# Kernel optimization log

Measured on AMD Instinct MI355X. Metric: run time of the kernel, lower is better.

The kernel has to match this reference:

```python
import jax, jax.numpy as jnp
import numpy as np

D_IN = 1024
D_OUT = 1024
H = 16            # head_cnt
G = 4             # attention_groups
LF = 2            # linformer_factor
HEAD_OUT = D_OUT // H          # 64 (value head dim)
DQ = HEAD_OUT // LF            # 32 (query/key head dim)
B, T = 2, 2048


def setup_inputs() -> dict:
    key = jax.random.key(0)
    ks = jax.random.split(key, 7)
    s = 0.02
    return {
        "x": jax.random.normal(ks[0], (B, T, D_IN), dtype=jnp.float32),
        "Wq": jax.random.normal(ks[1], (D_IN, D_OUT // LF), dtype=jnp.float32) * s,
        "Wk": jax.random.normal(ks[2], (D_IN, (D_OUT // LF) // G), dtype=jnp.float32) * s,
        "Wv": jax.random.normal(ks[3], (D_IN, D_OUT // G), dtype=jnp.float32) * s,
        "Wp": jax.random.normal(ks[4], (D_OUT, D_OUT), dtype=jnp.float32) * s,
        "bp": jnp.zeros((D_OUT,), dtype=jnp.float32),
    }


def _alibi_bias(T, dtype):
    # standard ALiBi slopes for H heads (H is a power of 2): m_h = 2^(-8h/H), h=1..H
    slopes = jnp.asarray(2.0 ** (-8.0 * np.arange(1, H + 1) / H), dtype=dtype)
    pos = jnp.arange(T)
    rel = (pos[None, :] - pos[:, None]).astype(dtype)  # j - i, <= 0 on causal part
    return slopes[:, None, None] * rel[None, :, :]      # (H, T, T)


def reference(x, Wq, Wk, Wv, Wp, bp):
    b, t, _ = x.shape
    q = x @ Wq                                  # (b, t, D_OUT/LF)
    k = jnp.tile(x @ Wk, (1, 1, G))             # repeat KV groups -> (b, t, D_OUT/LF)
    v = jnp.tile(x @ Wv, (1, 1, G))             # (b, t, D_OUT)

    q = q.reshape(b, t, H, DQ).transpose(0, 2, 1, 3)        # (b, H, t, DQ)
    k = k.reshape(b, t, H, DQ).transpose(0, 2, 1, 3)
    v = v.reshape(b, t, H, HEAD_OUT).transpose(0, 2, 1, 3)  # (b, H, t, HEAD_OUT)

    scores = jnp.einsum('bhqd,bhkd->bhqk', q, k)            # (b, H, t, t)
    causal = jnp.triu(jnp.ones((t, t), dtype=bool), k=1)
    scores = jnp.where(causal, -jnp.inf, scores)
    # faithful to source: alibi added after masking, then scaled by 1/sqrt(d_k)
    scores = (scores + _alibi_bias(t, scores.dtype)) / jnp.sqrt(jnp.asarray(DQ, scores.dtype))
    w = jax.nn.softmax(scores, axis=-1)
    ctx = jnp.einsum('bhqk,bhkd->bqhd', w, v).reshape(b, t, D_OUT)
    return ctx @ Wp + bp
```

## Files before the change

kernel.cpp:

```cpp
#include <hip/hip_runtime.h>
#include <hip/hip_bf16.h>

#define T_SEQ 2048
#define H_CNT 16
#define B_SZ  2
#define QKV_LD 896
#define KOFF   512
#define VOFF   640

typedef float  f32x4   __attribute__((ext_vector_type(4)));
typedef float  f32x16  __attribute__((ext_vector_type(16)));
typedef __bf16 bf16x8  __attribute__((ext_vector_type(8)));

static __device__ __forceinline__ ushort f2bf(float f) {
    union { float f; unsigned u; } v; v.f = f;
    unsigned u = v.u;
    unsigned r = (u + 0x7fffu + ((u >> 16) & 1u)) >> 16;
    return (ushort)r;
}
static __device__ __forceinline__ unsigned pack2bf(float a, float b) {
    union { __bf16 h[2]; unsigned u; } pk;
    pk.h[0] = (__bf16)a; pk.h[1] = (__bf16)b;
    return pk.u;
}

static __device__ __forceinline__ f32x4 mfma16(bf16x8 a, bf16x8 b, f32x4 c) {
    return __builtin_amdgcn_mfma_f32_16x16x32_bf16(a, b, c, 0, 0, 0);
}
static __device__ __forceinline__ f32x16 mfma32(bf16x8 a, bf16x8 b, f32x16 c) {
    return __builtin_amdgcn_mfma_f32_32x32x16_bf16(a, b, c, 0, 0, 0);
}

static __device__ __forceinline__ void gl_lds16(const void* g, void* l) {
    __builtin_amdgcn_global_load_lds((const __attribute__((address_space(1))) void*)g,
                                     (__attribute__((address_space(3))) void*)l, 16, 0, 0);
}

__global__ __launch_bounds__(256) void convert_bf16(const float* __restrict__ src,
                                                    ushort* __restrict__ dst) {
    const int i = blockIdx.x * 256 + threadIdx.x;
    const float4 v0 = reinterpret_cast<const float4*>(src)[i * 2];
    const float4 v1 = reinterpret_cast<const float4*>(src)[i * 2 + 1];
    uint4 o;
    o.x = (unsigned)f2bf(v0.x) | ((unsigned)f2bf(v0.y) << 16);
    o.y = (unsigned)f2bf(v0.z) | ((unsigned)f2bf(v0.w) << 16);
    o.z = (unsigned)f2bf(v1.x) | ((unsigned)f2bf(v1.y) << 16);
    o.w = (unsigned)f2bf(v1.z) | ((unsigned)f2bf(v1.w) << 16);
    reinterpret_cast<uint4*>(dst)[i] = o;
}

__global__ __launch_bounds__(256) void prep_weights(const float* __restrict__ Wq,
                                                    const float* __restrict__ Wk,
                                                    const float* __restrict__ Wv,
                                                    const float* __restrict__ Wp,
                                                    ushort* __restrict__ Wqkvt,
                                                    ushort* __restrict__ Wpt) {
    __shared__ float tile[32][33];
    const int x = blockIdx.x;
    const float* src; ushort* dst; int C, cx;
    if (x < 16)      { src = Wq; dst = Wqkvt;              C = 512;  cx = x; }
    else if (x < 20) { src = Wk; dst = Wqkvt + 512 * 1024; C = 128;  cx = x - 16; }
    else if (x < 28) { src = Wv; dst = Wqkvt + 640 * 1024; C = 256;  cx = x - 20; }
    else             { src = Wp; dst = Wpt;                C = 1024; cx = x - 28; }
    const int tx = threadIdx.x & 31, ty = threadIdx.x >> 5;
    const int r0 = blockIdx.y * 32, c0 = cx * 32;
#pragma unroll
    for (int i = 0; i < 32; i += 8)
        tile[ty + i][tx] = src[(size_t)(r0 + ty + i) * C + c0 + tx];
    __syncthreads();
#pragma unroll
    for (int i = 0; i < 32; i += 8)
        dst[(size_t)(c0 + ty + i) * 1024 + r0 + tx] = f2bf(tile[tx][ty + i]);
}

__global__ __launch_bounds__(256) void transpose_bf16_str(const ushort* __restrict__ src,
                                                          int src_ld, size_t src_zoff,
                                                          ushort* __restrict__ dst,
                                                          int R, int C, size_t dst_zoff) {
    __shared__ ushort tile[32][33];
    const int tx = threadIdx.x & 31, ty = threadIdx.x >> 5;
    const int r0 = blockIdx.y * 32, c0 = blockIdx.x * 32;
    const ushort* s = src + (size_t)blockIdx.z * src_zoff;
    ushort* d = dst + (size_t)blockIdx.z * dst_zoff;
#pragma unroll
    for (int i = 0; i < 32; i += 8)
        tile[ty + i][tx] = s[(size_t)(r0 + ty + i) * src_ld + c0 + tx];
    __syncthreads();
#pragma unroll
    for (int i = 0; i < 32; i += 8)
        d[(size_t)(c0 + ty + i) * R + r0 + tx] = tile[tx][ty + i];
}

template <bool OUT_BF16>
__global__ __launch_bounds__(256) void gemm_bf16(const ushort* __restrict__ A,
                                                 const ushort* __restrict__ Bt,
                                                 const float* __restrict__ bias,
                                                 void* __restrict__ Cout,
                                                 int M, int N, int K) {
    __shared__ __align__(16) ushort As[64 * 32];
    __shared__ __align__(16) ushort Bs[128 * 32];

    const int tid = threadIdx.x;
    const int w = tid >> 6, l = tid & 63;
    const int bm = blockIdx.y * 64, bn = blockIdx.x * 128;
    const int wr = (w >> 1) * 32, wc = (w & 1) * 64;
    const int lr = l & 15, lk = (l >> 4) * 8;
    const int crow = l >> 2, ck8 = (l & 3) * 8;

    const ushort* Ag0 = A + (size_t)(bm + w * 16 + crow) * K + ck8;
    const ushort* Bg0 = Bt + (size_t)(bn + w * 16 + crow) * K + ck8;
    const ushort* Bg1 = Bt + (size_t)(bn + (w + 4) * 16 + crow) * K + ck8;
    ushort* Al0 = &As[w * 16 * 32];
    ushort* Bl0 = &Bs[w * 16 * 32];
    ushort* Bl1 = &Bs[(w + 4) * 16 * 32];

    f32x4 acc[2][4];
#pragma unroll
    for (int m = 0; m < 2; ++m)
#pragma unroll
        for (int n = 0; n < 4; ++n) acc[m][n] = (f32x4){0.f, 0.f, 0.f, 0.f};

    for (int k0 = 0; k0 < K; k0 += 32) {
        __syncthreads();
        gl_lds16(Ag0 + k0, Al0);
        gl_lds16(Bg0 + k0, Bl0);
        gl_lds16(Bg1 + k0, Bl1);
        __syncthreads();

        bf16x8 af[2], bfr[4];
#pragma unroll
        for (int m = 0; m < 2; ++m)
            af[m] = *reinterpret_cast<const bf16x8*>(&As[(wr + m * 16 + lr) * 32 + lk]);
#pragma unroll
        for (int n = 0; n < 4; ++n)
            bfr[n] = *reinterpret_cast<const bf16x8*>(&Bs[(wc + n * 16 + lr) * 32 + lk]);
#pragma unroll
        for (int m = 0; m < 2; ++m)
#pragma unroll
            for (int n = 0; n < 4; ++n)
                acc[m][n] = mfma16(af[m], bfr[n], acc[m][n]);
    }

    const int orow = bm + wr + (l >> 4) * 4;
    const int ocol0 = bn + wc + lr;
#pragma unroll
    for (int m = 0; m < 2; ++m)
#pragma unroll
        for (int n = 0; n < 4; ++n) {
            const int col = ocol0 + n * 16;
            const float bv = OUT_BF16 ? 0.0f : bias[col];
#pragma unroll
            for (int r = 0; r < 4; ++r) {
                const size_t idx = (size_t)(orow + m * 16 + r) * N + col;
                if constexpr (OUT_BF16)
                    reinterpret_cast<ushort*>(Cout)[idx] = f2bf(acc[m][n][r]);
                else
                    reinterpret_cast<float*>(Cout)[idx] = acc[m][n][r] + bv;
            }
        }
}

#define LDK 40
#define LDV 72

__global__ __launch_bounds__(512) void attn_mfma7(const ushort* __restrict__ qkv,
                                                  const ushort* __restrict__ vT,
                                                  ushort* __restrict__ ctx) {
    __shared__ __align__(16) ushort Ks[2][64 * LDK];
    __shared__ __align__(16) ushort Vs[2][64 * LDV];
    __shared__ float lsred[4][32];

    const int tid = threadIdx.x;
    const int w = tid >> 6, l = tid & 63;
    const int lq = l & 31;
    const int hi = l >> 5;
    const int tp = blockIdx.x, g = blockIdx.y, b = blockIdx.z;
    const int hd = w & 3, grp = w >> 2;
    const int h = g + 4 * hd;

    const float slope = exp2f(-0.5f * (float)(h + 1));
    const float k1 = 0.17677669529663687f * 1.4426950408889634f;
    const float k2 = slope * k1;
    const int Wint = (int)(275.0f / slope);

    const int st = tid & 255;
    const int sd = st >> 2;
    const int c4 = st & 3;
    const int sc8 = c4 * 8;
    const int voff = (c4 & 1) * 4 + (c4 >> 1) * 16;
    const ushort* kgp = qkv + (size_t)b * T_SEQ * QKV_LD + KOFF + g * 32 + (size_t)sd * QKV_LD + sc8;
    const ushort* vgp = vT + ((size_t)b * 256 + g * 64 + sd) * T_SEQ;

    float* red = reinterpret_cast<float*>(&Vs[0][0]);

    int cur = 0;
    for (int ph = 0; ph < 2; ++ph) {
        const int t = ph ? tp : (63 - tp);
        const int i0 = t * 32;
        const int nkeys = i0 + 32;
        const int jtmax = (nkeys + 63) & ~63;

        const ushort* qrow = qkv + ((size_t)(b * T_SEQ + i0 + lq)) * QKV_LD + h * 32 + hi * 8;
        const bf16x8 qa = *reinterpret_cast<const bf16x8*>(qrow);
        const bf16x8 qb = *reinterpret_cast<const bf16x8*>(qrow + 16);

        f32x16 o0, o1;
#pragma unroll
        for (int r = 0; r < 16; ++r) { o0[r] = 0.0f; o1[r] = 0.0f; }
        float ls = 0.0f;

        uint4 kreg, vr0, vr1;
        if (tid < 256) {
            kreg = *reinterpret_cast<const uint4*>(kgp);
        } else {
            vr0 = *reinterpret_cast<const uint4*>(vgp + sc8);
            vr1 = *reinterpret_cast<const uint4*>(vgp + 32 + sc8);
        }

        for (int jt = 0; jt < jtmax; jt += 64) {
            if (tid < 256) {
                *reinterpret_cast<uint4*>(&Ks[cur][sd * LDK + sc8]) = kreg;
            } else {
                uint2 lo0 = make_uint2(vr0.x, vr0.y), hi0v = make_uint2(vr0.z, vr0.w);
                uint2 lo1 = make_uint2(vr1.x, vr1.y), hi1v = make_uint2(vr1.z, vr1.w);
                *reinterpret_cast<uint2*>(&Vs[cur][sd * LDV + voff]) = lo0;
                *reinterpret_cast<uint2*>(&Vs[cur][sd * LDV + voff + 8]) = hi0v;
                *reinterpret_cast<uint2*>(&Vs[cur][sd * LDV + 32 + voff]) = lo1;
                *reinterpret_cast<uint2*>(&Vs[cur][sd * LDV + 32 + voff + 8]) = hi1v;
            }
            const int jn = jt + 64;
            if (jn < jtmax) {
                if (tid < 256) {
                    kreg = *reinterpret_cast<const uint4*>(kgp + (size_t)jn * QKV_LD);
                } else {
                    vr0 = *reinterpret_cast<const uint4*>(vgp + jn + sc8);
                    vr1 = *reinterpret_cast<const uint4*>(vgp + jn + 32 + sc8);
                }
            }
            __syncthreads();

            const int jts = jt + 32 * grp;
            if (jts < nkeys && jts + 31 >= i0 - Wint) {
                const bf16x8 ka = *reinterpret_cast<const bf16x8*>(&Ks[cur][(32 * grp + lq) * LDK + hi * 8]);
                const bf16x8 kb2 = *reinterpret_cast<const bf16x8*>(&Ks[cur][(32 * grp + lq) * LDK + 16 + hi * 8]);
                f32x16 p;
#pragma unroll
                for (int r = 0; r < 16; ++r) p[r] = 0.0f;
                __builtin_amdgcn_s_setprio(1);
                p = mfma32(ka, qa, p);
                p = mfma32(kb2, qb, p);
                __builtin_amdgcn_s_setprio(0);

                const int dlt = jts + 4 * hi - i0 - lq;
                const float base2 = k2 * (float)dlt;
                float pe[16];
                if (jts + 31 > i0) {
#pragma unroll
                    for (int r = 0; r < 16; ++r) {
                        const int off = (r & 3) + 8 * (r >> 2);
                        const float arg = fmaf(p[r], k1, fmaf((float)off, k2, base2));
                        float e = exp2f(arg);
                        if (dlt + off > 0) e = 0.0f;
                        ls += e;
                        pe[r] = e;
                    }
                } else {
#pragma unroll
                    for (int r = 0; r < 16; ++r) {
                        const int off = (r & 3) + 8 * (r >> 2);
                        const float arg = fmaf(p[r], k1, fmaf((float)off, k2, base2));
                        const float e = exp2f(arg);
                        ls += e;
                        pe[r] = e;
                    }
                }
                union { unsigned u[4]; bf16x8 v; } A1, A2;
#pragma unroll
                for (int j2 = 0; j2 < 4; ++j2) A1.u[j2] = pack2bf(pe[2 * j2], pe[2 * j2 + 1]);
#pragma unroll
                for (int j2 = 0; j2 < 4; ++j2) A2.u[j2] = pack2bf(pe[8 + 2 * j2], pe[9 + 2 * j2]);

                const int vr0i = lq * LDV + 32 * grp;
                const int vr1i = (32 + lq) * LDV + 32 * grp;
                const bf16x8 v00 = *reinterpret_cast<const bf16x8*>(&Vs[cur][vr0i + hi * 8]);
                const bf16x8 v01 = *reinterpret_cast<const bf16x8*>(&Vs[cur][vr0i + 16 + hi * 8]);
                const bf16x8 v10 = *reinterpret_cast<const bf16x8*>(&Vs[cur][vr1i + hi * 8]);
                const bf16x8 v11 = *reinterpret_cast<const bf16x8*>(&Vs[cur][vr1i + 16 + hi * 8]);
                __builtin_amdgcn_s_setprio(1);
                o0 = mfma32(A1.v, v00, o0);
                o0 = mfma32(A2.v, v01, o0);
                o1 = mfma32(A1.v, v10, o1);
                o1 = mfma32(A2.v, v11, o1);
                __builtin_amdgcn_s_setprio(0);
            }
            cur ^= 1;
        }

        const float ls2 = ls + __shfl_xor(ls, 32);
        __syncthreads();
        if (grp == 0) {
#pragma unroll
            for (int r = 0; r < 16; ++r) red[hd * 1024 + l * 16 + r] = o0[r];
            if (hi == 0) lsred[hd][lq] = ls2;
        }
        __syncthreads();
        float inv = 0.0f;
        if (grp == 1) {
#pragma unroll
            for (int r = 0; r < 16; ++r) o0[r] += red[hd * 1024 + l * 16 + r];
            inv = 1.0f / (ls2 + lsred[hd][lq]);
        }
        __syncthreads();
        if (grp == 0) {
#pragma unroll
            for (int r = 0; r < 16; ++r) red[hd * 1024 + l * 16 + r] = o1[r];
        }
        __syncthreads();
        if (grp == 1) {
#pragma unroll
            for (int r = 0; r < 16; ++r) o1[r] += red[hd * 1024 + l * 16 + r];
#pragma unroll
            for (int r = 0; r < 16; ++r) {
                const int qr = (r & 3) + 8 * (r >> 2) + 4 * hi;
                const float invq = __shfl(inv, qr);
                const size_t row = (size_t)(b * T_SEQ + i0 + qr);
                ctx[row * 1024 + h * 64 + lq] = f2bf(o0[r] * invq);
                ctx[row * 1024 + h * 64 + 32 + lq] = f2bf(o1[r] * invq);
            }
        }
        __syncthreads();
    }
}

extern "C" void kernel_launch(void* const* d_in, const int* in_sizes, int n_in,
                              void* d_out, int out_size, void* d_ws, size_t ws_size,
                              hipStream_t stream) {
    const float* x  = (const float*)d_in[0];
    const float* Wq = (const float*)d_in[1];
    const float* Wk = (const float*)d_in[2];
    const float* Wv = (const float*)d_in[3];
    const float* Wp = (const float*)d_in[4];
    const float* bp = (const float*)d_in[5];

    const int M = B_SZ * T_SEQ;

    ushort* ws    = (ushort*)d_ws;
    ushort* xb    = ws;
    ushort* Wqkvt = xb + 4194304;
    ushort* Wpt   = Wqkvt + 917504;
    ushort* qkv   = Wpt + 1048576;
    ushort* vTb   = qkv + 3670016;
    ushort* cbuf  = vTb + 1048576;

    convert_bf16<<<2048, 256, 0, stream>>>(x, xb);
    prep_weights<<<dim3(60, 32), 256, 0, stream>>>(Wq, Wk, Wv, Wp, Wqkvt, Wpt);

    gemm_bf16<true><<<dim3(7, 64), 256, 0, stream>>>(xb, Wqkvt, nullptr, qkv, M, 896, 1024);

    transpose_bf16_str<<<dim3(8, 64, 2), 256, 0, stream>>>(
        qkv + VOFF, QKV_LD, (size_t)T_SEQ * QKV_LD, vTb, T_SEQ, 256, (size_t)256 * T_SEQ);

    attn_mfma7<<<dim3(32, 4, B_SZ), 512, 0, stream>>>(qkv, vTb, cbuf);

    gemm_bf16<false><<<dim3(8, 64), 256, 0, stream>>>(cbuf, Wpt, bp, (float*)d_out, M, 1024, 1024);
}
```

Measured before the change: 100.5 us.

## Widen attention to 16 waves with 4-way key split; double GEMM k-step

The attention kernel now launches 1024 threads per block. Each head's key range is split across four wave groups using 128-key tiles, with a three-slot LDS reduction for the partial outputs and row sums. This raises in-flight waves per CU, since the grid only fills about one block per CU. The GEMM loads two 32-wide K slices per barrier pair, halving sync count per K. The costs are higher reduction overhead and more idle waves on short causal rows.

```diff
diff --git a/kernel.cpp b/kernel.cpp
--- a/kernel.cpp
+++ b/kernel.cpp
@@ -97,8 +97,8 @@
                                                  const float* __restrict__ bias,
                                                  void* __restrict__ Cout,
                                                  int M, int N, int K) {
-    __shared__ __align__(16) ushort As[64 * 32];
-    __shared__ __align__(16) ushort Bs[128 * 32];
+    __shared__ __align__(16) ushort Aa[64 * 32], Ab[64 * 32];
+    __shared__ __align__(16) ushort Ba[128 * 32], Bb[128 * 32];
 
     const int tid = threadIdx.x;
     const int w = tid >> 6, l = tid & 63;
@@ -107,12 +107,15 @@
     const int lr = l & 15, lk = (l >> 4) * 8;
     const int crow = l >> 2, ck8 = (l & 3) * 8;
 
-    const ushort* Ag0 = A + (size_t)(bm + w * 16 + crow) * K + ck8;
+    const ushort* Ag  = A + (size_t)(bm + w * 16 + crow) * K + ck8;
     const ushort* Bg0 = Bt + (size_t)(bn + w * 16 + crow) * K + ck8;
     const ushort* Bg1 = Bt + (size_t)(bn + (w + 4) * 16 + crow) * K + ck8;
-    ushort* Al0 = &As[w * 16 * 32];
-    ushort* Bl0 = &Bs[w * 16 * 32];
-    ushort* Bl1 = &Bs[(w + 4) * 16 * 32];
+    ushort* Ala  = &Aa[w * 16 * 32];
+    ushort* Alb  = &Ab[w * 16 * 32];
+    ushort* Bl0a = &Ba[w * 16 * 32];
+    ushort* Bl0b = &Bb[w * 16 * 32];
+    ushort* Bl1a = &Ba[(w + 4) * 16 * 32];
+    ushort* Bl1b = &Bb[(w + 4) * 16 * 32];
 
     f32x4 acc[2][4];
 #pragma unroll
@@ -120,25 +123,34 @@
 #pragma unroll
         for (int n = 0; n < 4; ++n) acc[m][n] = (f32x4){0.f, 0.f, 0.f, 0.f};
 
-    for (int k0 = 0; k0 < K; k0 += 32) {
-        __syncthreads();
-        gl_lds16(Ag0 + k0, Al0);
-        gl_lds16(Bg0 + k0, Bl0);
-        gl_lds16(Bg1 + k0, Bl1);
-        __syncthreads();
-
-        bf16x8 af[2], bfr[4];
+    for (int k0 = 0; k0 < K; k0 += 64) {
+        __syncthreads();
+        gl_lds16(Ag + k0, Ala);
+        gl_lds16(Ag + k0 + 32, Alb);
+        gl_lds16(Bg0 + k0, Bl0a);
+        gl_lds16(Bg0 + k0 + 32, Bl0b);
+        gl_lds16(Bg1 + k0, Bl1a);
+        gl_lds16(Bg1 + k0 + 32, Bl1b);
+        __syncthreads();
+
+        bf16x8 af0[2], af1[2], bf0[4], bf1[4];
+#pragma unroll
+        for (int m = 0; m < 2; ++m) {
+            af0[m] = *reinterpret_cast<const bf16x8*>(&Aa[(wr + m * 16 + lr) * 32 + lk]);
+            af1[m] = *reinterpret_cast<const bf16x8*>(&Ab[(wr + m * 16 + lr) * 32 + lk]);
+        }
+#pragma unroll
+        for (int n = 0; n < 4; ++n) {
+            bf0[n] = *reinterpret_cast<const bf16x8*>(&Ba[(wc + n * 16 + lr) * 32 + lk]);
+            bf1[n] = *reinterpret_cast<const bf16x8*>(&Bb[(wc + n * 16 + lr) * 32 + lk]);
+        }
 #pragma unroll
         for (int m = 0; m < 2; ++m)
-            af[m] = *reinterpret_cast<const bf16x8*>(&As[(wr + m * 16 + lr) * 32 + lk]);
-#pragma unroll
-        for (int n = 0; n < 4; ++n)
-            bfr[n] = *reinterpret_cast<const bf16x8*>(&Bs[(wc + n * 16 + lr) * 32 + lk]);
-#pragma unroll
-        for (int m = 0; m < 2; ++m)
-#pragma unroll
-            for (int n = 0; n < 4; ++n)
-                acc[m][n] = mfma16(af[m], bfr[n], acc[m][n]);
+#pragma unroll
+            for (int n = 0; n < 4; ++n) {
+                acc[m][n] = mfma16(af0[m], bf0[n], acc[m][n]);
+                acc[m][n] = mfma16(af1[m], bf1[n], acc[m][n]);
+            }
     }
 
     const int orow = bm + wr + (l >> 4) * 4;
@@ -161,14 +173,14 @@
 }
 
 #define LDK 40
-#define LDV 72
-
-__global__ __launch_bounds__(512) void attn_mfma7(const ushort* __restrict__ qkv,
-                                                  const ushort* __restrict__ vT,
-                                                  ushort* __restrict__ ctx) {
-    __shared__ __align__(16) ushort Ks[2][64 * LDK];
+#define LDV 136
+
+__global__ __launch_bounds__(1024) void attn_mfma8(const ushort* __restrict__ qkv,
+                                                   const ushort* __restrict__ vT,
+                                                   ushort* __restrict__ ctx) {
+    __shared__ __align__(16) ushort Ks[2][128 * LDK];
     __shared__ __align__(16) ushort Vs[2][64 * LDV];
-    __shared__ float lsred[4][32];
+    __shared__ float lsred[3][4][32];
 
     const int tid = threadIdx.x;
     const int w = tid >> 6, l = tid & 63;
@@ -183,22 +195,28 @@
     const float k2 = slope * k1;
     const int Wint = (int)(275.0f / slope);
 
-    const int st = tid & 255;
-    const int sd = st >> 2;
-    const int c4 = st & 3;
-    const int sc8 = c4 * 8;
-    const int voff = (c4 & 1) * 4 + (c4 >> 1) * 16;
-    const ushort* kgp = qkv + (size_t)b * T_SEQ * QKV_LD + KOFF + g * 32 + (size_t)sd * QKV_LD + sc8;
-    const ushort* vgp = vT + ((size_t)b * 256 + g * 64 + sd) * T_SEQ;
-
-    float* red = reinterpret_cast<float*>(&Vs[0][0]);
+    const int ksd = tid >> 2, kc4 = tid & 3;
+    const ushort* kgp = qkv + (size_t)b * T_SEQ * QKV_LD + KOFF + g * 32 +
+                        (size_t)ksd * QKV_LD + kc4 * 8;
+    const int sv = tid & 511;
+    const int vsd = sv >> 3, vj = sv & 7;
+    const int vs0 = (vj >> 2) << 1, vc4 = vj & 3;
+    const int voff = (vc4 & 1) * 4 + (vc4 >> 1) * 16;
+    const ushort* vgp = vT + ((size_t)b * 256 + g * 64 + vsd) * T_SEQ + vs0 * 32 + vc4 * 8;
+    const int vl0 = vsd * LDV + vs0 * 32 + voff;
+    const int vl1 = vsd * LDV + (vs0 + 1) * 32 + voff;
+
+    float* slotA = reinterpret_cast<float*>(&Ks[0][0]);
+    float* slotB = reinterpret_cast<float*>(&Vs[0][0]);
+    float* slotC = reinterpret_cast<float*>(&Vs[1][0]);
+    const int sidx = (hd * 64 + l) * 16;
 
     int cur = 0;
     for (int ph = 0; ph < 2; ++ph) {
         const int t = ph ? tp : (63 - tp);
         const int i0 = t * 32;
         const int nkeys = i0 + 32;
-        const int jtmax = (nkeys + 63) & ~63;
+        const int jtmax = (nkeys + 127) & ~127;
 
         const ushort* qrow = qkv + ((size_t)(b * T_SEQ + i0 + lq)) * QKV_LD + h * 32 + hi * 8;
         const bf16x8 qa = *reinterpret_cast<const bf16x8*>(qrow);
@@ -210,39 +228,37 @@
         float ls = 0.0f;
 
         uint4 kreg, vr0, vr1;
-        if (tid < 256) {
+        if (tid < 512) {
             kreg = *reinterpret_cast<const uint4*>(kgp);
         } else {
-            vr0 = *reinterpret_cast<const uint4*>(vgp + sc8);
-            vr1 = *reinterpret_cast<const uint4*>(vgp + 32 + sc8);
-        }
-
-        for (int jt = 0; jt < jtmax; jt += 64) {
-            if (tid < 256) {
-                *reinterpret_cast<uint4*>(&Ks[cur][sd * LDK + sc8]) = kreg;
+            vr0 = *reinterpret_cast<const uint4*>(vgp);
+            vr1 = *reinterpret_cast<const uint4*>(vgp + 32);
+        }
+
+        for (int jt = 0; jt < jtmax; jt += 128) {
+            if (tid < 512) {
+                *reinterpret_cast<uint4*>(&Ks[cur][ksd * LDK + kc4 * 8]) = kreg;
             } else {
-                uint2 lo0 = make_uint2(vr0.x, vr0.y), hi0v = make_uint2(vr0.z, vr0.w);
-                uint2 lo1 = make_uint2(vr1.x, vr1.y), hi1v = make_uint2(vr1.z, vr1.w);
-                *reinterpret_cast<uint2*>(&Vs[cur][sd * LDV + voff]) = lo0;
-                *reinterpret_cast<uint2*>(&Vs[cur][sd * LDV + voff + 8]) = hi0v;
-                *reinterpret_cast<uint2*>(&Vs[cur][sd * LDV + 32 + voff]) = lo1;
-                *reinterpret_cast<uint2*>(&Vs[cur][sd * LDV + 32 + voff + 8]) = hi1v;
-            }
-            const int jn = jt + 64;
+                *reinterpret_cast<uint2*>(&Vs[cur][vl0]) = make_uint2(vr0.x, vr0.y);
+                *reinterpret_cast<uint2*>(&Vs[cur][vl0 + 8]) = make_uint2(vr0.z, vr0.w);
+                *reinterpret_cast<uint2*>(&Vs[cur][vl1]) = make_uint2(vr1.x, vr1.y);
+                *reinterpret_cast<uint2*>(&Vs[cur][vl1 + 8]) = make_uint2(vr1.z, vr1.w);
+            }
+            const int jn = jt + 128;
             if (jn < jtmax) {
-                if (tid < 256) {
+                if (tid < 512) {
                     kreg = *reinterpret_cast<const uint4*>(kgp + (size_t)jn * QKV_LD);
                 } else {
-                    vr0 = *reinterpret_cast<const uint4*>(vgp + jn + sc8);
-                    vr1 = *reinterpret_cast<const uint4*>(vgp + jn + 32 + sc8);
+                    vr0 = *reinterpret_cast<const uint4*>(vgp + jn);
+                    vr1 = *reinterpret_cast<const uint4*>(vgp + jn + 32);
                 }
             }
             __syncthreads();
 
             const int jts = jt + 32 * grp;
             if (jts < nkeys && jts + 31 >= i0 - Wint) {
-                const bf16x8 ka = *reinterpret_cast<const bf16x8*>(&Ks[cur][(32 * grp + lq) * LDK + hi * 8]);
-                const bf16x8 kb2 = *reinterpret_cast<const bf16x8*>(&Ks[cur][(32 * grp + lq) * LDK + 16 + hi * 8]);
+                const bf16x8 ka = *reinterpret_cast<const bf16x8*>(&Ks[cur][(grp * 32 + lq) * LDK + hi * 8]);
+                const bf16x8 kb2 = *reinterpret_cast<const bf16x8*>(&Ks[cur][(grp * 32 + lq) * LDK + 16 + hi * 8]);
                 f32x16 p;
 #pragma unroll
                 for (int r = 0; r < 16; ++r) p[r] = 0.0f;
@@ -280,8 +296,8 @@
 #pragma unroll
                 for (int j2 = 0; j2 < 4; ++j2) A2.u[j2] = pack2bf(pe[8 + 2 * j2], pe[9 + 2 * j2]);
 
-                const int vr0i = lq * LDV + 32 * grp;
-                const int vr1i = (32 + lq) * LDV + 32 * grp;
+                const int vr0i = lq * LDV + grp * 32;
+                const int vr1i = (32 + lq) * LDV + grp * 32;
                 const bf16x8 v00 = *reinterpret_cast<const bf16x8*>(&Vs[cur][vr0i + hi * 8]);
                 const bf16x8 v01 = *reinterpret_cast<const bf16x8*>(&Vs[cur][vr0i + 16 + hi * 8]);
                 const bf16x8 v10 = *reinterpret_cast<const bf16x8*>(&Vs[cur][vr1i + hi * 8]);
@@ -298,27 +314,31 @@
 
         const float ls2 = ls + __shfl_xor(ls, 32);
         __syncthreads();
+        if (grp) {
+            float* sl = (grp == 1) ? slotA : (grp == 2) ? slotB : slotC;
+#pragma unroll
+            for (int r = 0; r < 16; ++r) sl[sidx + r] = o0[r];
+            if (hi == 0) lsred[grp - 1][hd][lq] = ls2;
+        }
+        __syncthreads();
+        float inv = 0.0f;
         if (grp == 0) {
 #pragma unroll
-            for (int r = 0; r < 16; ++r) red[hd * 1024 + l * 16 + r] = o0[r];
-            if (hi == 0) lsred[hd][lq] = ls2;
-        }
-        __syncthreads();
-        float inv = 0.0f;
-        if (grp == 1) {
-#pragma unroll
-            for (int r = 0; r < 16; ++r) o0[r] += red[hd * 1024 + l * 16 + r];
-            inv = 1.0f / (ls2 + lsred[hd][lq]);
+            for (int r = 0; r < 16; ++r)
+                o0[r] += slotA[sidx + r] + slotB[sidx + r] + slotC[sidx + r];
+            inv = 1.0f / (ls2 + lsred[0][hd][lq] + lsred[1][hd][lq] + lsred[2][hd][lq]);
+        }
+        __syncthreads();
+        if (grp) {
+            float* sl = (grp == 1) ? slotA : (grp == 2) ? slotB : slotC;
+#pragma unroll
+            for (int r = 0; r < 16; ++r) sl[sidx + r] = o1[r];
         }
         __syncthreads();
         if (grp == 0) {
 #pragma unroll
-            for (int r = 0; r < 16; ++r) red[hd * 1024 + l * 16 + r] = o1[r];
-        }
-        __syncthreads();
-        if (grp == 1) {
-#pragma unroll
-            for (int r = 0; r < 16; ++r) o1[r] += red[hd * 1024 + l * 16 + r];
+            for (int r = 0; r < 16; ++r)
+                o1[r] += slotA[sidx + r] + slotB[sidx + r] + slotC[sidx + r];
 #pragma unroll
             for (int r = 0; r < 16; ++r) {
                 const int qr = (r & 3) + 8 * (r >> 2) + 4 * hi;
@@ -360,7 +380,7 @@
     transpose_bf16_str<<<dim3(8, 64, 2), 256, 0, stream>>>(
         qkv + VOFF, QKV_LD, (size_t)T_SEQ * QKV_LD, vTb, T_SEQ, 256, (size_t)256 * T_SEQ);
 
-    attn_mfma7<<<dim3(32, 4, B_SZ), 512, 0, stream>>>(qkv, vTb, cbuf);
+    attn_mfma8<<<dim3(32, 4, B_SZ), 1024, 0, stream>>>(qkv, vTb, cbuf);
 
     gemm_bf16<false><<<dim3(8, 64), 256, 0, stream>>>(cbuf, Wpt, bp, (float*)d_out, M, 1024, 1024);
 }
```

Result: no change. 100.9 us (+0.4%).
